# Optimization experiments

Measured on AMD Instinct MI355X. Metric: run time of the kernel, lower is better.

## Reference

```python
import jax, jax.numpy as jnp
import numpy as np

N = 4096        # number of nodes
C = 512         # in_features
L_LAT = 64      # L_latent
EPS = 0.25      # epsilon


def setup_inputs() -> dict:
    key = jax.random.key(0)
    ks = jax.random.split(key, 8)
    def lin(k, fan_in, shape):
        return (jax.random.normal(k, shape, jnp.float32) / np.float32(np.sqrt(fan_in)))
    x = jax.random.normal(ks[0], (N, C), jnp.float32)
    adj = jax.random.uniform(ks[1], (N, N), jnp.float32)  # dense nonneg kernel
    W_proj = lin(ks[2], C, (C, L_LAT)); b_proj = jnp.zeros((L_LAT,), jnp.float32)
    W_pi1 = lin(ks[3], L_LAT, (L_LAT, C)); b_pi1 = jnp.zeros((C,), jnp.float32)
    W_pi2 = lin(ks[4], C, (C, 1)); b_pi2 = jnp.zeros((1,), jnp.float32)
    W_f = lin(ks[5], C, (C, C)); b_f = jnp.zeros((C,), jnp.float32)
    dt = jnp.array([0.1], jnp.float32)
    return {"x": x, "adj": adj, "W_proj": W_proj, "b_proj": b_proj,
            "W_pi1": W_pi1, "b_pi1": b_pi1, "W_pi2": W_pi2, "b_pi2": b_pi2,
            "W_f": W_f, "b_f": b_f, "dt": dt}


def reference(x, adj, W_proj, b_proj, W_pi1, b_pi1, W_pi2, b_pi2, W_f, b_f, dt):
    # proj_list: x -> latent [n, L]
    z = x @ W_proj + b_proj
    # pi_list: Linear -> ReLU -> Linear -> Sigmoid, squeeze to [n]
    pi = jax.nn.sigmoid(jax.nn.relu(z @ W_pi1 + b_pi1) @ W_pi2 + b_pi2)[:, 0]
    # q_epsilon_tilde: row sums of the kernel
    q = adj.sum(axis=1)                       # [n]
    # K_tilde = K_epsilon @ diag(pi/q)  == column scaling
    K_tilde = adj * (pi / q)[None, :]         # [n, n]
    # D_tilde diagonal; torch.inverse of a diagonal == elementwise reciprocal
    d = K_tilde.sum(axis=1) + 1e-5            # [n]
    # target = relu(f(x)) with f = Linear(C, C)
    target = jax.nn.relu(x @ W_f + b_f)       # [n, C]
    # L @ target = (1/eps) * diag(1/d) @ K_tilde @ target - target
    Lt = (K_tilde @ target) / (EPS * d)[:, None] - target
    return target + dt[0] * Lt
```

## Files before the change

kernel.cpp:

```cpp
#include <hip/hip_runtime.h>
#include <hip/hip_bf16.h>

#define N_NODES 4096
#define C_DIM   512
#define L_DIM   64

typedef unsigned short u16;
using bf16x8 = __attribute__((ext_vector_type(8))) __bf16;
using u16x8  = __attribute__((ext_vector_type(8))) unsigned short;
using f32x4  = __attribute__((ext_vector_type(4))) float;

__device__ __forceinline__ float b2f(u16 u) {
    union { unsigned int i; float f; } v; v.i = ((unsigned int)u) << 16; return v.f;
}
__device__ __forceinline__ u16 f2b(float f) {
    unsigned int u = __float_as_uint(f);
    u += 0x7fff + ((u >> 16) & 1);
    return (u16)(u >> 16);
}

__device__ __forceinline__ void gload16(const u16* g, u16* l) {
    __builtin_amdgcn_global_load_lds((const __attribute__((address_space(1))) void*)g,
                                     (__attribute__((address_space(3))) void*)l,
                                     16, 0, 0);
}

__device__ __forceinline__ int detect_mode_inl(const u16* __restrict__ adj) {
    int m = 0;
#pragma unroll
    for (int i = 0; i < 64; ++i) m |= (adj[i] >= 0x8000) ? 1 : 0;
    return m;
}

#define OFF_DT    64
#define OFF_BIAS  1024
#define OFF_WP    4096
#define OFF_BP    135168
#define OFF_WP1   135424
#define OFF_BP1   266496
#define OFF_WP2   268544
#define OFF_BP2   270592
#define OFF_Q     271360
#define OFF_S     287744
#define OFF_DV    304128
#define OFF_T     1048576
#define OFF_TST   9437184
#define OFF_WFT   13631488
#define OFF_XB    14155776
#define OFF_ADJB  18350080

__device__ __forceinline__ float ldin(const void* p, int i, int mode) {
    if (mode) return ((const float*)p)[i];
    return b2f(((const u16*)p)[i]);
}

__global__ __launch_bounds__(256) void convert_params(const u16* __restrict__ adjdet,
        const void* Wp, const void* bp, const void* Wp1, const void* bp1,
        const void* Wp2, const void* bp2, const void* bfc, const void* dt,
        float* Wp_f, float* bp_f, float* Wp1_f, float* bp1_f,
        float* Wp2_f, float* bp2_f, float* bias_f, float* dt_f) {
    int idx = blockIdx.x * 256 + threadIdx.x;
    int mode = detect_mode_inl(adjdet);
    if (idx < 32768)        Wp_f[idx]          = ldin(Wp,  idx, mode);
    else if (idx < 32832)   bp_f[idx - 32768]  = ldin(bp,  idx - 32768, mode);
    else if (idx < 65600)   Wp1_f[idx - 32832] = ldin(Wp1, idx - 32832, mode);
    else if (idx < 66112)   bp1_f[idx - 65600] = ldin(bp1, idx - 65600, mode);
    else if (idx < 66624)   Wp2_f[idx - 66112] = ldin(Wp2, idx - 66112, mode);
    else if (idx == 66624)  bp2_f[0]           = ldin(bp2, 0, mode);
    else if (idx < 67137)   bias_f[idx - 66625] = ldin(bfc, idx - 66625, mode);
    else if (idx == 67137)  dt_f[0]            = ldin(dt, 0, mode);
}

__global__ __launch_bounds__(256) void prep_x(const void* __restrict__ xraw,
                                              const u16* __restrict__ adjdet,
                                              u16* __restrict__ xb) {
    if (detect_mode_inl(adjdet) == 0) return;
    int idx = blockIdx.x * 256 + threadIdx.x;
    float4 v = ((const float4*)xraw)[idx];
    ushort4 o; o.x = f2b(v.x); o.y = f2b(v.y); o.z = f2b(v.z); o.w = f2b(v.w);
    ((ushort4*)xb)[idx] = o;
}

__global__ __launch_bounds__(256) void prep_adj(const void* __restrict__ adjraw,
                                                u16* __restrict__ adjb,
                                                float* __restrict__ q) {
    int mode = detect_mode_inl((const u16*)adjraw);
    int wave = threadIdx.x >> 6, lane = threadIdx.x & 63;
    int row = blockIdx.x * 4 + wave;
    float acc = 0.f;
    if (mode) {
        const float4* rp = (const float4*)((const float*)adjraw + (size_t)row * N_NODES);
        ushort4* wp = (ushort4*)(adjb + (size_t)row * N_NODES);
#pragma unroll
        for (int it = 0; it < 16; ++it) {
            float4 v = rp[it * 64 + lane];
            acc += v.x + v.y + v.z + v.w;
            ushort4 o; o.x = f2b(v.x); o.y = f2b(v.y); o.z = f2b(v.z); o.w = f2b(v.w);
            wp[it * 64 + lane] = o;
        }
    } else {
        const u16x8* rp = (const u16x8*)((const u16*)adjraw + (size_t)row * N_NODES);
#pragma unroll
        for (int it = 0; it < 8; ++it) {
            u16x8 v = rp[it * 64 + lane];
#pragma unroll
            for (int e = 0; e < 8; ++e) acc += b2f(v[e]);
        }
    }
#pragma unroll
    for (int off = 32; off > 0; off >>= 1) acc += __shfl_down(acc, off);
    if (lane == 0) q[row] = acc;
}

__global__ __launch_bounds__(256) void pi_kernel(const void* __restrict__ xraw,
                                                 const u16* __restrict__ adjdet,
                                                 const float* __restrict__ Wp_f,  const float* __restrict__ bp_f,
                                                 const float* __restrict__ Wp1_f, const float* __restrict__ bp1_f,
                                                 const float* __restrict__ Wp2_f, const float* __restrict__ bp2_f,
                                                 const float* __restrict__ q, float* __restrict__ s) {
    __shared__ float sx[8][C_DIM];
    __shared__ float sz[8][L_DIM];
    __shared__ float red[4][8];
    int tid = threadIdx.x;
    int i0 = blockIdx.x * 8;
    int mode = detect_mode_inl(adjdet);
    if (mode) {
        const float4* xp = (const float4*)((const float*)xraw + (size_t)i0 * C_DIM);
        float4* sxf = (float4*)&sx[0][0];
#pragma unroll
        for (int r = 0; r < 4; ++r) sxf[tid + 256 * r] = xp[tid + 256 * r];
    } else {
        const u16x8* xp = (const u16x8*)((const u16*)xraw + (size_t)i0 * C_DIM);
#pragma unroll
        for (int r = 0; r < 2; ++r) {
            u16x8 v = xp[tid + 256 * r];
            float* dstf = &sx[0][0] + (size_t)(tid + 256 * r) * 8;
#pragma unroll
            for (int e = 0; e < 8; ++e) dstf[e] = b2f(v[e]);
        }
    }
    __syncthreads();
    int j = tid & 63, n0 = tid >> 6;
    float a0 = 0.f, a1 = 0.f;
#pragma unroll 4
    for (int k = 0; k < C_DIM; ++k) {
        float w = Wp_f[k * L_DIM + j];
        a0 += sx[n0][k] * w;
        a1 += sx[n0 + 4][k] * w;
    }
    sz[n0][j] = a0 + bp_f[j];
    sz[n0 + 4][j] = a1 + bp_f[j];
    __syncthreads();
    int m0 = tid, m1 = tid + 256;
    float b0 = bp1_f[m0], b1 = bp1_f[m1];
    float h0[8], h1[8];
#pragma unroll
    for (int n = 0; n < 8; ++n) { h0[n] = b0; h1[n] = b1; }
#pragma unroll 8
    for (int jj = 0; jj < L_DIM; ++jj) {
        float w0 = Wp1_f[jj * C_DIM + m0];
        float w1 = Wp1_f[jj * C_DIM + m1];
#pragma unroll
        for (int n = 0; n < 8; ++n) {
            float z = sz[n][jj];
            h0[n] += z * w0;
            h1[n] += z * w1;
        }
    }
    float w2a = Wp2_f[m0], w2b = Wp2_f[m1];
    float p[8];
#pragma unroll
    for (int n = 0; n < 8; ++n)
        p[n] = fmaxf(h0[n], 0.f) * w2a + fmaxf(h1[n], 0.f) * w2b;
#pragma unroll
    for (int off = 32; off > 0; off >>= 1)
#pragma unroll
        for (int n = 0; n < 8; ++n) p[n] += __shfl_down(p[n], off);
    int lane = tid & 63, wave = tid >> 6;
    if (lane == 0) {
#pragma unroll
        for (int n = 0; n < 8; ++n) red[wave][n] = p[n];
    }
    __syncthreads();
    if (tid < 8) {
        float tot = red[0][tid] + red[1][tid] + red[2][tid] + red[3][tid] + bp2_f[0];
        float pi = 1.f / (1.f + expf(-tot));
        s[i0 + tid] = pi / q[i0 + tid];
    }
}

__global__ __launch_bounds__(256) void dvec_kernel(const void* __restrict__ adjraw,
                                                   const u16* __restrict__ adjb,
                                                   const float* __restrict__ s,
                                                   float* __restrict__ d) {
    int mode = detect_mode_inl((const u16*)adjraw);
    const u16* A = mode ? adjb : (const u16*)adjraw;
    int wave = threadIdx.x >> 6, lane = threadIdx.x & 63;
    int row = blockIdx.x * 4 + wave;
    const u16x8* rp = (const u16x8*)(A + (size_t)row * N_NODES);
    float acc = 0.f;
#pragma unroll
    for (int it = 0; it < 8; ++it) {
        int chunk = it * 64 + lane;
        u16x8 v = rp[chunk];
        const float4* sp = (const float4*)(s + chunk * 8);
        float4 s0 = sp[0], s1 = sp[1];
        acc += b2f(v[0]) * s0.x + b2f(v[1]) * s0.y + b2f(v[2]) * s0.z + b2f(v[3]) * s0.w;
        acc += b2f(v[4]) * s1.x + b2f(v[5]) * s1.y + b2f(v[6]) * s1.z + b2f(v[7]) * s1.w;
    }
#pragma unroll
    for (int off = 32; off > 0; off >>= 1) acc += __shfl_down(acc, off);
    if (lane == 0) d[row] = acc + 1e-5f;
}

__global__ __launch_bounds__(256) void trans_Wf(const void* __restrict__ Wfraw,
                                                const u16* __restrict__ adjdet,
                                                u16* __restrict__ WfT) {
    __shared__ float tile[32][33];
    int mode = detect_mode_inl(adjdet);
    int tx = threadIdx.x, ty = threadIdx.y;
    int x0 = blockIdx.x * 32, y0 = blockIdx.y * 32;
    if (mode) {
        const float* src = (const float*)Wfraw;
#pragma unroll
        for (int r = ty; r < 32; r += 8) tile[r][tx] = src[(size_t)(y0 + r) * C_DIM + x0 + tx];
    } else {
        const u16* src = (const u16*)Wfraw;
#pragma unroll
        for (int r = ty; r < 32; r += 8) tile[r][tx] = b2f(src[(size_t)(y0 + r) * C_DIM + x0 + tx]);
    }
    __syncthreads();
#pragma unroll
    for (int r = ty; r < 32; r += 8)
        WfT[(size_t)(x0 + r) * C_DIM + y0 + tx] = f2b(tile[tx][r]);
}

__global__ __launch_bounds__(256) void trans_scale(const float* __restrict__ T,
                                                   const float* __restrict__ s,
                                                   u16* __restrict__ dst) {
    __shared__ float tile[32][33];
    int tx = threadIdx.x, ty = threadIdx.y;
    int x0 = blockIdx.x * 32, y0 = blockIdx.y * 32;
#pragma unroll
    for (int r = ty; r < 32; r += 8) tile[r][tx] = T[(size_t)(y0 + r) * C_DIM + x0 + tx];
    __syncthreads();
    float sv = s[y0 + tx];
#pragma unroll
    for (int r = ty; r < 32; r += 8)
        dst[(size_t)(x0 + r) * N_NODES + y0 + tx] = f2b(tile[tx][r] * sv);
}

template <int EPI>
__global__ __launch_bounds__(256) void gemm_tile(const u16* __restrict__ adjdet,
                                                 const u16* __restrict__ Abf, const u16* __restrict__ Aalt,
                                                 const u16* __restrict__ BT, int K,
                                                 float* __restrict__ T, const float* __restrict__ dvec,
                                                 const float* __restrict__ bias_f, const float* __restrict__ dt_f,
                                                 void* __restrict__ out) {
    __shared__ __align__(16) u16 lA[64 * 32];
    __shared__ __align__(16) u16 lB[64 * 32];
    int mode = detect_mode_inl(adjdet);
    const u16* A = mode ? Aalt : Abf;
    int tid = threadIdx.x;
    int lane = tid & 63, wave = tid >> 6;
    int bm = blockIdx.x * 64, bn = blockIdx.y * 64;
    int quad = lane >> 4, l15 = lane & 15;
    int wm = wave * 16;

    const u16* Ap = A + (size_t)(bm + (tid >> 2)) * K + (tid & 3) * 8;
    const u16* Bp = BT + (size_t)(bn + (tid >> 2)) * K + (tid & 3) * 8;
    u16* la = lA + tid * 8;
    u16* lb = lB + tid * 8;

    f32x4 acc[4];
#pragma unroll
    for (int nt = 0; nt < 4; ++nt) acc[nt] = (f32x4){0.f, 0.f, 0.f, 0.f};

    for (int k0 = 0; k0 < K; k0 += 32) {
        gload16(Ap + k0, la);
        gload16(Bp + k0, lb);
        __syncthreads();
        bf16x8 af = *(const bf16x8*)&lA[(wm + l15) * 32 + quad * 8];
        bf16x8 bfv[4];
#pragma unroll
        for (int nt = 0; nt < 4; ++nt) bfv[nt] = *(const bf16x8*)&lB[(nt * 16 + l15) * 32 + quad * 8];
#pragma unroll
        for (int nt = 0; nt < 4; ++nt)
            acc[nt] = __builtin_amdgcn_mfma_f32_16x16x32_bf16(af, bfv[nt], acc[nt], 0, 0, 0);
        __syncthreads();
    }

    if (EPI == 1) {
#pragma unroll
        for (int nt = 0; nt < 4; ++nt) {
            int col = bn + nt * 16 + l15;
            float bv = bias_f[col];
#pragma unroll
            for (int r = 0; r < 4; ++r) {
                int row = bm + wm + quad * 4 + r;
                T[(size_t)row * C_DIM + col] = fmaxf(acc[nt][r] + bv, 0.f);
            }
        }
    } else {
        float dtv = dt_f[0];
        float c0 = 1.f - dtv;
        float c1 = dtv * 4.f;
#pragma unroll
        for (int nt = 0; nt < 4; ++nt) {
            int col = bn + nt * 16 + l15;
#pragma unroll
            for (int r = 0; r < 4; ++r) {
                int row = bm + wm + quad * 4 + r;
                float t = T[(size_t)row * C_DIM + col];
                float val = c0 * t + c1 * acc[nt][r] / dvec[row];
                if (mode) ((float*)out)[(size_t)row * C_DIM + col] = val;
                else      ((u16*)out)[(size_t)row * C_DIM + col] = f2b(val);
            }
        }
    }
}

extern "C" void kernel_launch(void* const* d_in, const int* in_sizes, int n_in,
                              void* d_out, int out_size, void* d_ws, size_t ws_size,
                              hipStream_t stream) {
    const void* x   = d_in[0];
    const void* adj = d_in[1];
    const void* Wp  = d_in[2];
    const void* bp  = d_in[3];
    const void* Wp1 = d_in[4];
    const void* bp1 = d_in[5];
    const void* Wp2 = d_in[6];
    const void* bp2 = d_in[7];
    const void* Wf  = d_in[8];
    const void* bfc = d_in[9];
    const void* dtp = d_in[10];
    const u16* adjdet = (const u16*)adj;

    char* ws = (char*)d_ws;
    float* dt_f   = (float*)(ws + OFF_DT);
    float* bias_f = (float*)(ws + OFF_BIAS);
    float* Wp_f   = (float*)(ws + OFF_WP);
    float* bp_f   = (float*)(ws + OFF_BP);
    float* Wp1_f  = (float*)(ws + OFF_WP1);
    float* bp1_f  = (float*)(ws + OFF_BP1);
    float* Wp2_f  = (float*)(ws + OFF_WP2);
    float* bp2_f  = (float*)(ws + OFF_BP2);
    float* q      = (float*)(ws + OFF_Q);
    float* s      = (float*)(ws + OFF_S);
    float* dv     = (float*)(ws + OFF_DV);
    float* T      = (float*)(ws + OFF_T);
    u16*   TsT    = (u16*)(ws + OFF_TST);
    u16*   WfT    = (u16*)(ws + OFF_WFT);
    u16*   xb     = (u16*)(ws + OFF_XB);
    u16*   adjb   = (u16*)(ws + OFF_ADJB);

    convert_params<<<263, 256, 0, stream>>>(adjdet, Wp, bp, Wp1, bp1, Wp2, bp2, bfc, dtp,
                                            Wp_f, bp_f, Wp1_f, bp1_f, Wp2_f, bp2_f, bias_f, dt_f);
    prep_x<<<2048, 256, 0, stream>>>(x, adjdet, xb);
    prep_adj<<<N_NODES / 4, 256, 0, stream>>>(adj, adjb, q);
    pi_kernel<<<N_NODES / 8, 256, 0, stream>>>(x, adjdet, Wp_f, bp_f, Wp1_f, bp1_f, Wp2_f, bp2_f, q, s);
    dvec_kernel<<<N_NODES / 4, 256, 0, stream>>>(adj, adjb, s, dv);
    trans_Wf<<<dim3(16, 16), dim3(32, 8), 0, stream>>>(Wf, adjdet, WfT);
    gemm_tile<1><<<dim3(N_NODES / 64, C_DIM / 64), 256, 0, stream>>>(
        adjdet, (const u16*)x, xb, WfT, C_DIM, T, nullptr, bias_f, nullptr, nullptr);
    trans_scale<<<dim3(16, 128), dim3(32, 8), 0, stream>>>(T, s, TsT);
    gemm_tile<2><<<dim3(N_NODES / 64, C_DIM / 64), 256, 0, stream>>>(
        adjdet, (const u16*)adj, adjb, TsT, N_NODES, T, dv, nullptr, dt_f, d_out);
}
```

Measured before the change: 253.5 us.

## Merge launches into five fused kernels and split-K the adjacency GEMM with atomics

Nine launches are merged into five multi-role kernels: parameter, x, adjacency and Wf prep share one launch, pi and the first GEMM share one, and the d-vector, transpose-scale and output init share one. The big adjacency GEMM now uses 128x64 tiles split four ways along K, and partial results are atomically added into an output pre-filled with (1-dt)*T. A final kernel converts the accumulator to bf16 when the input is bf16. This cuts launch gaps and gives the main GEMM more parallelism, at the cost of atomic traffic and a non-deterministic summation order.

```diff
diff --git a/kernel.cpp b/kernel.cpp
--- a/kernel.cpp
+++ b/kernel.cpp
@@ -4,6 +4,8 @@
 #define N_NODES 4096
 #define C_DIM   512
 #define L_DIM   64
+#define SPLITS  4
+#define KCHUNK  (N_NODES / SPLITS)
 
 typedef unsigned short u16;
 using bf16x8 = __attribute__((ext_vector_type(8))) __bf16;
@@ -54,243 +56,186 @@
     return b2f(((const u16*)p)[i]);
 }
 
-__global__ __launch_bounds__(256) void convert_params(const u16* __restrict__ adjdet,
+__global__ __launch_bounds__(256) void k1_prep(const void* __restrict__ adj, const void* __restrict__ x,
         const void* Wp, const void* bp, const void* Wp1, const void* bp1,
-        const void* Wp2, const void* bp2, const void* bfc, const void* dt,
-        float* Wp_f, float* bp_f, float* Wp1_f, float* bp1_f,
-        float* Wp2_f, float* bp2_f, float* bias_f, float* dt_f) {
-    int idx = blockIdx.x * 256 + threadIdx.x;
+        const void* Wp2, const void* bp2, const void* Wf, const void* bfc, const void* dt,
+        float* __restrict__ Wp_f, float* __restrict__ bp_f, float* __restrict__ Wp1_f,
+        float* __restrict__ bp1_f, float* __restrict__ Wp2_f, float* __restrict__ bp2_f,
+        float* __restrict__ bias_f, float* __restrict__ dt_f,
+        u16* __restrict__ adjb, float* __restrict__ q, u16* __restrict__ xb,
+        u16* __restrict__ WfT) {
+    __shared__ float tile[32][33];
+    int bid = blockIdx.x, tid = threadIdx.x;
+    int mode = detect_mode_inl((const u16*)adj);
+    if (bid < 263) {
+        int idx = bid * 256 + tid;
+        if (idx < 32768)        Wp_f[idx]          = ldin(Wp,  idx, mode);
+        else if (idx < 32832)   bp_f[idx - 32768]  = ldin(bp,  idx - 32768, mode);
+        else if (idx < 65600)   Wp1_f[idx - 32832] = ldin(Wp1, idx - 32832, mode);
+        else if (idx < 66112)   bp1_f[idx - 65600] = ldin(bp1, idx - 65600, mode);
+        else if (idx < 66624)   Wp2_f[idx - 66112] = ldin(Wp2, idx - 66112, mode);
+        else if (idx == 66624)  bp2_f[0]           = ldin(bp2, 0, mode);
+        else if (idx < 67137)   bias_f[idx - 66625] = ldin(bfc, idx - 66625, mode);
+        else if (idx == 67137)  dt_f[0]            = ldin(dt, 0, mode);
+    } else if (bid < 2311) {
+        if (mode == 0) return;
+        int idx = (bid - 263) * 256 + tid;
+        float4 v = ((const float4*)x)[idx];
+        ushort4 o; o.x = f2b(v.x); o.y = f2b(v.y); o.z = f2b(v.z); o.w = f2b(v.w);
+        ((ushort4*)xb)[idx] = o;
+    } else if (bid < 3335) {
+        int wave = tid >> 6, lane = tid & 63;
+        int row = (bid - 2311) * 4 + wave;
+        float acc = 0.f;
+        if (mode) {
+            const float4* rp = (const float4*)((const float*)adj + (size_t)row * N_NODES);
+            ushort4* wp = (ushort4*)(adjb + (size_t)row * N_NODES);
+#pragma unroll
+            for (int it = 0; it < 16; ++it) {
+                float4 v = rp[it * 64 + lane];
+                acc += v.x + v.y + v.z + v.w;
+                ushort4 o; o.x = f2b(v.x); o.y = f2b(v.y); o.z = f2b(v.z); o.w = f2b(v.w);
+                wp[it * 64 + lane] = o;
+            }
+        } else {
+            const u16x8* rp = (const u16x8*)((const u16*)adj + (size_t)row * N_NODES);
+#pragma unroll
+            for (int it = 0; it < 8; ++it) {
+                u16x8 v = rp[it * 64 + lane];
+#pragma unroll
+                for (int e = 0; e < 8; ++e) acc += b2f(v[e]);
+            }
+        }
+#pragma unroll
+        for (int off = 32; off > 0; off >>= 1) acc += __shfl_down(acc, off);
+        if (lane == 0) q[row] = acc;
+    } else {
+        int g = bid - 3335;
+        int tx = tid & 31, ty = tid >> 5;
+        int x0 = (g & 15) * 32, y0 = (g >> 4) * 32;
+        if (mode) {
+            const float* src = (const float*)Wf;
+#pragma unroll
+            for (int r = ty; r < 32; r += 8) tile[r][tx] = src[(size_t)(y0 + r) * C_DIM + x0 + tx];
+        } else {
+            const u16* src = (const u16*)Wf;
+#pragma unroll
+            for (int r = ty; r < 32; r += 8) tile[r][tx] = b2f(src[(size_t)(y0 + r) * C_DIM + x0 + tx]);
+        }
+        __syncthreads();
+#pragma unroll
+        for (int r = ty; r < 32; r += 8)
+            WfT[(size_t)(x0 + r) * C_DIM + y0 + tx] = f2b(tile[tx][r]);
+    }
+}
+
+__global__ __launch_bounds__(256) void k2_pi_gemm1(const void* __restrict__ xraw,
+        const u16* __restrict__ adjdet, const u16* __restrict__ xb, const u16* __restrict__ WfT,
+        const float* __restrict__ Wp_f,  const float* __restrict__ bp_f,
+        const float* __restrict__ Wp1_f, const float* __restrict__ bp1_f,
+        const float* __restrict__ Wp2_f, const float* __restrict__ bp2_f,
+        const float* __restrict__ bias_f,
+        const float* __restrict__ q, float* __restrict__ s, float* __restrict__ T) {
+    __shared__ __align__(16) char smem[18560];
+    int bid = blockIdx.x, tid = threadIdx.x;
     int mode = detect_mode_inl(adjdet);
-    if (idx < 32768)        Wp_f[idx]          = ldin(Wp,  idx, mode);
-    else if (idx < 32832)   bp_f[idx - 32768]  = ldin(bp,  idx - 32768, mode);
-    else if (idx < 65600)   Wp1_f[idx - 32832] = ldin(Wp1, idx - 32832, mode);
-    else if (idx < 66112)   bp1_f[idx - 65600] = ldin(bp1, idx - 65600, mode);
-    else if (idx < 66624)   Wp2_f[idx - 66112] = ldin(Wp2, idx - 66112, mode);
-    else if (idx == 66624)  bp2_f[0]           = ldin(bp2, 0, mode);
-    else if (idx < 67137)   bias_f[idx - 66625] = ldin(bfc, idx - 66625, mode);
-    else if (idx == 67137)  dt_f[0]            = ldin(dt, 0, mode);
-}
-
-__global__ __launch_bounds__(256) void prep_x(const void* __restrict__ xraw,
-                                              const u16* __restrict__ adjdet,
-                                              u16* __restrict__ xb) {
-    if (detect_mode_inl(adjdet) == 0) return;
-    int idx = blockIdx.x * 256 + threadIdx.x;
-    float4 v = ((const float4*)xraw)[idx];
-    ushort4 o; o.x = f2b(v.x); o.y = f2b(v.y); o.z = f2b(v.z); o.w = f2b(v.w);
-    ((ushort4*)xb)[idx] = o;
-}
-
-__global__ __launch_bounds__(256) void prep_adj(const void* __restrict__ adjraw,
-                                                u16* __restrict__ adjb,
-                                                float* __restrict__ q) {
-    int mode = detect_mode_inl((const u16*)adjraw);
-    int wave = threadIdx.x >> 6, lane = threadIdx.x & 63;
-    int row = blockIdx.x * 4 + wave;
-    float acc = 0.f;
-    if (mode) {
-        const float4* rp = (const float4*)((const float*)adjraw + (size_t)row * N_NODES);
-        ushort4* wp = (ushort4*)(adjb + (size_t)row * N_NODES);
-#pragma unroll
-        for (int it = 0; it < 16; ++it) {
-            float4 v = rp[it * 64 + lane];
-            acc += v.x + v.y + v.z + v.w;
-            ushort4 o; o.x = f2b(v.x); o.y = f2b(v.y); o.z = f2b(v.z); o.w = f2b(v.w);
-            wp[it * 64 + lane] = o;
+    if (bid < 512) {
+        float (*sx)[C_DIM] = (float(*)[C_DIM])smem;
+        float (*sz)[L_DIM] = (float(*)[L_DIM])(smem + 16384);
+        float (*red)[8]    = (float(*)[8])(smem + 18432);
+        int i0 = bid * 8;
+        if (mode) {
+            const float4* xp = (const float4*)((const float*)xraw + (size_t)i0 * C_DIM);
+            float4* sxf = (float4*)&sx[0][0];
+#pragma unroll
+            for (int r = 0; r < 4; ++r) sxf[tid + 256 * r] = xp[tid + 256 * r];
+        } else {
+            const u16x8* xp = (const u16x8*)((const u16*)xraw + (size_t)i0 * C_DIM);
+#pragma unroll
+            for (int r = 0; r < 2; ++r) {
+                u16x8 v = xp[tid + 256 * r];
+                float* dstf = &sx[0][0] + (size_t)(tid + 256 * r) * 8;
+#pragma unroll
+                for (int e = 0; e < 8; ++e) dstf[e] = b2f(v[e]);
+            }
+        }
+        __syncthreads();
+        int j = tid & 63, n0 = tid >> 6;
+        float a0 = 0.f, a1 = 0.f;
+#pragma unroll 4
+        for (int k = 0; k < C_DIM; ++k) {
+            float w = Wp_f[k * L_DIM + j];
+            a0 += sx[n0][k] * w;
+            a1 += sx[n0 + 4][k] * w;
+        }
+        sz[n0][j] = a0 + bp_f[j];
+        sz[n0 + 4][j] = a1 + bp_f[j];
+        __syncthreads();
+        int m0 = tid, m1 = tid + 256;
+        float b0 = bp1_f[m0], b1 = bp1_f[m1];
+        float h0[8], h1[8];
+#pragma unroll
+        for (int n = 0; n < 8; ++n) { h0[n] = b0; h1[n] = b1; }
+#pragma unroll 8
+        for (int jj = 0; jj < L_DIM; ++jj) {
+            float w0 = Wp1_f[jj * C_DIM + m0];
+            float w1 = Wp1_f[jj * C_DIM + m1];
+#pragma unroll
+            for (int n = 0; n < 8; ++n) {
+                float z = sz[n][jj];
+                h0[n] += z * w0;
+                h1[n] += z * w1;
+            }
+        }
+        float w2a = Wp2_f[m0], w2b = Wp2_f[m1];
+        float p[8];
+#pragma unroll
+        for (int n = 0; n < 8; ++n)
+            p[n] = fmaxf(h0[n], 0.f) * w2a + fmaxf(h1[n], 0.f) * w2b;
+#pragma unroll
+        for (int off = 32; off > 0; off >>= 1)
+#pragma unroll
+            for (int n = 0; n < 8; ++n) p[n] += __shfl_down(p[n], off);
+        int lane = tid & 63, wave = tid >> 6;
+        if (lane == 0) {
+#pragma unroll
+            for (int n = 0; n < 8; ++n) red[wave][n] = p[n];
+        }
+        __syncthreads();
+        if (tid < 8) {
+            float tot = red[0][tid] + red[1][tid] + red[2][tid] + red[3][tid] + bp2_f[0];
+            float pi = 1.f / (1.f + expf(-tot));
+            s[i0 + tid] = pi / q[i0 + tid];
         }
     } else {
-        const u16x8* rp = (const u16x8*)((const u16*)adjraw + (size_t)row * N_NODES);
-#pragma unroll
-        for (int it = 0; it < 8; ++it) {
-            u16x8 v = rp[it * 64 + lane];
-#pragma unroll
-            for (int e = 0; e < 8; ++e) acc += b2f(v[e]);
-        }
-    }
-#pragma unroll
-    for (int off = 32; off > 0; off >>= 1) acc += __shfl_down(acc, off);
-    if (lane == 0) q[row] = acc;
-}
-
-__global__ __launch_bounds__(256) void pi_kernel(const void* __restrict__ xraw,
-                                                 const u16* __restrict__ adjdet,
-                                                 const float* __restrict__ Wp_f,  const float* __restrict__ bp_f,
-                                                 const float* __restrict__ Wp1_f, const float* __restrict__ bp1_f,
-                                                 const float* __restrict__ Wp2_f, const float* __restrict__ bp2_f,
-                                                 const float* __restrict__ q, float* __restrict__ s) {
-    __shared__ float sx[8][C_DIM];
-    __shared__ float sz[8][L_DIM];
-    __shared__ float red[4][8];
-    int tid = threadIdx.x;
-    int i0 = blockIdx.x * 8;
-    int mode = detect_mode_inl(adjdet);
-    if (mode) {
-        const float4* xp = (const float4*)((const float*)xraw + (size_t)i0 * C_DIM);
-        float4* sxf = (float4*)&sx[0][0];
-#pragma unroll
-        for (int r = 0; r < 4; ++r) sxf[tid + 256 * r] = xp[tid + 256 * r];
-    } else {
-        const u16x8* xp = (const u16x8*)((const u16*)xraw + (size_t)i0 * C_DIM);
-#pragma unroll
-        for (int r = 0; r < 2; ++r) {
-            u16x8 v = xp[tid + 256 * r];
-            float* dstf = &sx[0][0] + (size_t)(tid + 256 * r) * 8;
-#pragma unroll
-            for (int e = 0; e < 8; ++e) dstf[e] = b2f(v[e]);
-        }
-    }
-    __syncthreads();
-    int j = tid & 63, n0 = tid >> 6;
-    float a0 = 0.f, a1 = 0.f;
-#pragma unroll 4
-    for (int k = 0; k < C_DIM; ++k) {
-        float w = Wp_f[k * L_DIM + j];
-        a0 += sx[n0][k] * w;
-        a1 += sx[n0 + 4][k] * w;
-    }
-    sz[n0][j] = a0 + bp_f[j];
-    sz[n0 + 4][j] = a1 + bp_f[j];
-    __syncthreads();
-    int m0 = tid, m1 = tid + 256;
-    float b0 = bp1_f[m0], b1 = bp1_f[m1];
-    float h0[8], h1[8];
-#pragma unroll
-    for (int n = 0; n < 8; ++n) { h0[n] = b0; h1[n] = b1; }
-#pragma unroll 8
-    for (int jj = 0; jj < L_DIM; ++jj) {
-        float w0 = Wp1_f[jj * C_DIM + m0];
-        float w1 = Wp1_f[jj * C_DIM + m1];
-#pragma unroll
-        for (int n = 0; n < 8; ++n) {
-            float z = sz[n][jj];
-            h0[n] += z * w0;
-            h1[n] += z * w1;
-        }
-    }
-    float w2a = Wp2_f[m0], w2b = Wp2_f[m1];
-    float p[8];
-#pragma unroll
-    for (int n = 0; n < 8; ++n)
-        p[n] = fmaxf(h0[n], 0.f) * w2a + fmaxf(h1[n], 0.f) * w2b;
-#pragma unroll
-    for (int off = 32; off > 0; off >>= 1)
-#pragma unroll
-        for (int n = 0; n < 8; ++n) p[n] += __shfl_down(p[n], off);
-    int lane = tid & 63, wave = tid >> 6;
-    if (lane == 0) {
-#pragma unroll
-        for (int n = 0; n < 8; ++n) red[wave][n] = p[n];
-    }
-    __syncthreads();
-    if (tid < 8) {
-        float tot = red[0][tid] + red[1][tid] + red[2][tid] + red[3][tid] + bp2_f[0];
-        float pi = 1.f / (1.f + expf(-tot));
-        s[i0 + tid] = pi / q[i0 + tid];
-    }
-}
-
-__global__ __launch_bounds__(256) void dvec_kernel(const void* __restrict__ adjraw,
-                                                   const u16* __restrict__ adjb,
-                                                   const float* __restrict__ s,
-                                                   float* __restrict__ d) {
-    int mode = detect_mode_inl((const u16*)adjraw);
-    const u16* A = mode ? adjb : (const u16*)adjraw;
-    int wave = threadIdx.x >> 6, lane = threadIdx.x & 63;
-    int row = blockIdx.x * 4 + wave;
-    const u16x8* rp = (const u16x8*)(A + (size_t)row * N_NODES);
-    float acc = 0.f;
-#pragma unroll
-    for (int it = 0; it < 8; ++it) {
-        int chunk = it * 64 + lane;
-        u16x8 v = rp[chunk];
-        const float4* sp = (const float4*)(s + chunk * 8);
-        float4 s0 = sp[0], s1 = sp[1];
-        acc += b2f(v[0]) * s0.x + b2f(v[1]) * s0.y + b2f(v[2]) * s0.z + b2f(v[3]) * s0.w;
-        acc += b2f(v[4]) * s1.x + b2f(v[5]) * s1.y + b2f(v[6]) * s1.z + b2f(v[7]) * s1.w;
-    }
-#pragma unroll
-    for (int off = 32; off > 0; off >>= 1) acc += __shfl_down(acc, off);
-    if (lane == 0) d[row] = acc + 1e-5f;
-}
-
-__global__ __launch_bounds__(256) void trans_Wf(const void* __restrict__ Wfraw,
-                                                const u16* __restrict__ adjdet,
-                                                u16* __restrict__ WfT) {
-    __shared__ float tile[32][33];
-    int mode = detect_mode_inl(adjdet);
-    int tx = threadIdx.x, ty = threadIdx.y;
-    int x0 = blockIdx.x * 32, y0 = blockIdx.y * 32;
-    if (mode) {
-        const float* src = (const float*)Wfraw;
-#pragma unroll
-        for (int r = ty; r < 32; r += 8) tile[r][tx] = src[(size_t)(y0 + r) * C_DIM + x0 + tx];
-    } else {
-        const u16* src = (const u16*)Wfraw;
-#pragma unroll
-        for (int r = ty; r < 32; r += 8) tile[r][tx] = b2f(src[(size_t)(y0 + r) * C_DIM + x0 + tx]);
-    }
-    __syncthreads();
-#pragma unroll
-    for (int r = ty; r < 32; r += 8)
-        WfT[(size_t)(x0 + r) * C_DIM + y0 + tx] = f2b(tile[tx][r]);
-}
-
-__global__ __launch_bounds__(256) void trans_scale(const float* __restrict__ T,
-                                                   const float* __restrict__ s,
-                                                   u16* __restrict__ dst) {
-    __shared__ float tile[32][33];
-    int tx = threadIdx.x, ty = threadIdx.y;
-    int x0 = blockIdx.x * 32, y0 = blockIdx.y * 32;
-#pragma unroll
-    for (int r = ty; r < 32; r += 8) tile[r][tx] = T[(size_t)(y0 + r) * C_DIM + x0 + tx];
-    __syncthreads();
-    float sv = s[y0 + tx];
-#pragma unroll
-    for (int r = ty; r < 32; r += 8)
-        dst[(size_t)(x0 + r) * N_NODES + y0 + tx] = f2b(tile[tx][r] * sv);
-}
-
-template <int EPI>
-__global__ __launch_bounds__(256) void gemm_tile(const u16* __restrict__ adjdet,
-                                                 const u16* __restrict__ Abf, const u16* __restrict__ Aalt,
-                                                 const u16* __restrict__ BT, int K,
-                                                 float* __restrict__ T, const float* __restrict__ dvec,
-                                                 const float* __restrict__ bias_f, const float* __restrict__ dt_f,
-                                                 void* __restrict__ out) {
-    __shared__ __align__(16) u16 lA[64 * 32];
-    __shared__ __align__(16) u16 lB[64 * 32];
-    int mode = detect_mode_inl(adjdet);
-    const u16* A = mode ? Aalt : Abf;
-    int tid = threadIdx.x;
-    int lane = tid & 63, wave = tid >> 6;
-    int bm = blockIdx.x * 64, bn = blockIdx.y * 64;
-    int quad = lane >> 4, l15 = lane & 15;
-    int wm = wave * 16;
-
-    const u16* Ap = A + (size_t)(bm + (tid >> 2)) * K + (tid & 3) * 8;
-    const u16* Bp = BT + (size_t)(bn + (tid >> 2)) * K + (tid & 3) * 8;
-    u16* la = lA + tid * 8;
-    u16* lb = lB + tid * 8;
-
-    f32x4 acc[4];
-#pragma unroll
-    for (int nt = 0; nt < 4; ++nt) acc[nt] = (f32x4){0.f, 0.f, 0.f, 0.f};
-
-    for (int k0 = 0; k0 < K; k0 += 32) {
-        gload16(Ap + k0, la);
-        gload16(Bp + k0, lb);
-        __syncthreads();
-        bf16x8 af = *(const bf16x8*)&lA[(wm + l15) * 32 + quad * 8];
-        bf16x8 bfv[4];
-#pragma unroll
-        for (int nt = 0; nt < 4; ++nt) bfv[nt] = *(const bf16x8*)&lB[(nt * 16 + l15) * 32 + quad * 8];
-#pragma unroll
-        for (int nt = 0; nt < 4; ++nt)
-            acc[nt] = __builtin_amdgcn_mfma_f32_16x16x32_bf16(af, bfv[nt], acc[nt], 0, 0, 0);
-        __syncthreads();
-    }
-
-    if (EPI == 1) {
+        u16* lA = (u16*)smem;
+        u16* lB = (u16*)(smem + 4096);
+        const u16* A = mode ? xb : (const u16*)xraw;
+        int g = bid - 512;
+        int lane = tid & 63, wave = tid >> 6;
+        int bm = (g & 63) * 64, bn = (g >> 6) * 64;
+        int quad = lane >> 4, l15 = lane & 15;
+        int wm = wave * 16;
+        const u16* Ap = A + (size_t)(bm + (tid >> 2)) * C_DIM + (tid & 3) * 8;
+        const u16* Bp = WfT + (size_t)(bn + (tid >> 2)) * C_DIM + (tid & 3) * 8;
+        u16* la = lA + tid * 8;
+        u16* lb = lB + tid * 8;
+        f32x4 acc[4];
+#pragma unroll
+        for (int nt = 0; nt < 4; ++nt) acc[nt] = (f32x4){0.f, 0.f, 0.f, 0.f};
+        for (int k0 = 0; k0 < C_DIM; k0 += 32) {
+            gload16(Ap + k0, la);
+            gload16(Bp + k0, lb);
+            __syncthreads();
+            bf16x8 af = *(const bf16x8*)&lA[(wm + l15) * 32 + quad * 8];
+            bf16x8 bfv[4];
+#pragma unroll
+            for (int nt = 0; nt < 4; ++nt) bfv[nt] = *(const bf16x8*)&lB[(nt * 16 + l15) * 32 + quad * 8];
+#pragma unroll
+            for (int nt = 0; nt < 4; ++nt)
+                acc[nt] = __builtin_amdgcn_mfma_f32_16x16x32_bf16(af, bfv[nt], acc[nt], 0, 0, 0);
+            __syncthreads();
+        }
 #pragma unroll
         for (int nt = 0; nt < 4; ++nt) {
             int col = bn + nt * 16 + l15;
@@ -301,23 +246,128 @@
                 T[(size_t)row * C_DIM + col] = fmaxf(acc[nt][r] + bv, 0.f);
             }
         }
+    }
+}
+
+__global__ __launch_bounds__(256) void k3_mid(const void* __restrict__ adjraw,
+        const u16* __restrict__ adjb, const float* __restrict__ s,
+        const float* __restrict__ T, const float* __restrict__ dt_f,
+        float* __restrict__ dv, u16* __restrict__ TsT,
+        void* __restrict__ out, float* __restrict__ Pacc) {
+    __shared__ float tile[32][33];
+    int bid = blockIdx.x, tid = threadIdx.x;
+    int mode = detect_mode_inl((const u16*)adjraw);
+    if (bid < 1024) {
+        const u16* A = mode ? adjb : (const u16*)adjraw;
+        int wave = tid >> 6, lane = tid & 63;
+        int row = bid * 4 + wave;
+        const u16x8* rp = (const u16x8*)(A + (size_t)row * N_NODES);
+        float acc = 0.f;
+#pragma unroll
+        for (int it = 0; it < 8; ++it) {
+            int chunk = it * 64 + lane;
+            u16x8 v = rp[chunk];
+            const float4* sp = (const float4*)(s + chunk * 8);
+            float4 s0 = sp[0], s1 = sp[1];
+            acc += b2f(v[0]) * s0.x + b2f(v[1]) * s0.y + b2f(v[2]) * s0.z + b2f(v[3]) * s0.w;
+            acc += b2f(v[4]) * s1.x + b2f(v[5]) * s1.y + b2f(v[6]) * s1.z + b2f(v[7]) * s1.w;
+        }
+#pragma unroll
+        for (int off = 32; off > 0; off >>= 1) acc += __shfl_down(acc, off);
+        if (lane == 0) dv[row] = acc + 1e-5f;
+    } else if (bid < 3072) {
+        int g = bid - 1024;
+        int tx = tid & 31, ty = tid >> 5;
+        int x0 = (g & 15) * 32, y0 = (g >> 4) * 32;
+#pragma unroll
+        for (int r = ty; r < 32; r += 8) tile[r][tx] = T[(size_t)(y0 + r) * C_DIM + x0 + tx];
+        __syncthreads();
+        float sv = s[y0 + tx];
+#pragma unroll
+        for (int r = ty; r < 32; r += 8)
+            TsT[(size_t)(x0 + r) * N_NODES + y0 + tx] = f2b(tile[tx][r] * sv);
     } else {
-        float dtv = dt_f[0];
-        float c0 = 1.f - dtv;
-        float c1 = dtv * 4.f;
+        int idx = (bid - 3072) * 256 + tid;
+        float c0 = 1.f - dt_f[0];
+        float4 t = ((const float4*)T)[idx];
+        float4 v; v.x = c0 * t.x; v.y = c0 * t.y; v.z = c0 * t.z; v.w = c0 * t.w;
+        float* tgt = mode ? (float*)out : Pacc;
+        ((float4*)tgt)[idx] = v;
+    }
+}
+
+__global__ __launch_bounds__(256) void k4_gemm2(const void* __restrict__ adjraw,
+        const u16* __restrict__ adjb, const u16* __restrict__ TsT,
+        const float* __restrict__ dv, const float* __restrict__ dt_f,
+        void* __restrict__ out, float* __restrict__ Pacc) {
+    __shared__ __align__(16) u16 lA[128 * 32];
+    __shared__ __align__(16) u16 lB[64 * 32];
+    int mode = detect_mode_inl((const u16*)adjraw);
+    const u16* A = mode ? adjb : (const u16*)adjraw;
+    float* tgt = mode ? (float*)out : Pacc;
+    int tid = threadIdx.x;
+    int lane = tid & 63, wave = tid >> 6;
+    int bm = blockIdx.x * 128, bn = blockIdx.y * 64;
+    int kbase = blockIdx.z * KCHUNK;
+    int quad = lane >> 4, l15 = lane & 15;
+    int wm = wave * 32;
+
+    const u16* Ab0 = A + (size_t)(bm + (tid >> 2)) * N_NODES + kbase + (tid & 3) * 8;
+    const u16* Ab1 = A + (size_t)(bm + 64 + (tid >> 2)) * N_NODES + kbase + (tid & 3) * 8;
+    const u16* Bp  = TsT + (size_t)(bn + (tid >> 2)) * N_NODES + kbase + (tid & 3) * 8;
+    u16* la0 = lA + tid * 8;  u16* la1 = lA + 2048 + tid * 8;
+    u16* lb  = lB + tid * 8;
+
+    f32x4 acc[2][4];
+#pragma unroll
+    for (int a = 0; a < 2; ++a)
+#pragma unroll
+        for (int b = 0; b < 4; ++b) acc[a][b] = (f32x4){0.f, 0.f, 0.f, 0.f};
+
+    for (int k0 = 0; k0 < KCHUNK; k0 += 32) {
+        gload16(Ab0 + k0, la0);
+        gload16(Ab1 + k0, la1);
+        gload16(Bp + k0, lb);
+        __syncthreads();
+        bf16x8 af[2], bfv[4];
+#pragma unroll
+        for (int mt = 0; mt < 2; ++mt) af[mt] = *(const bf16x8*)&lA[(wm + mt * 16 + l15) * 32 + quad * 8];
+#pragma unroll
+        for (int nt = 0; nt < 4; ++nt) bfv[nt] = *(const bf16x8*)&lB[(nt * 16 + l15) * 32 + quad * 8];
+#pragma unroll
+        for (int mt = 0; mt < 2; ++mt)
+#pragma unroll
+            for (int nt = 0; nt < 4; ++nt)
+                acc[mt][nt] = __builtin_amdgcn_mfma_f32_16x16x32_bf16(af[mt], bfv[nt], acc[mt][nt], 0, 0, 0);
+        __syncthreads();
+    }
+
+    float c1 = dt_f[0] * 4.f;
+#pragma unroll
+    for (int mt = 0; mt < 2; ++mt) {
+        float inv[4];
+#pragma unroll
+        for (int r = 0; r < 4; ++r) inv[r] = c1 / dv[bm + wm + mt * 16 + quad * 4 + r];
 #pragma unroll
         for (int nt = 0; nt < 4; ++nt) {
             int col = bn + nt * 16 + l15;
 #pragma unroll
             for (int r = 0; r < 4; ++r) {
-                int row = bm + wm + quad * 4 + r;
-                float t = T[(size_t)row * C_DIM + col];
-                float val = c0 * t + c1 * acc[nt][r] / dvec[row];
-                if (mode) ((float*)out)[(size_t)row * C_DIM + col] = val;
-                else      ((u16*)out)[(size_t)row * C_DIM + col] = f2b(val);
+                int row = bm + wm + mt * 16 + quad * 4 + r;
+                atomicAdd(&tgt[(size_t)row * C_DIM + col], acc[mt][nt][r] * inv[r]);
             }
         }
     }
+}
+
+__global__ __launch_bounds__(256) void k5_fin(const void* __restrict__ adjraw,
+                                              const float* __restrict__ Pacc,
+                                              u16* __restrict__ out) {
+    if (detect_mode_inl((const u16*)adjraw)) return;
+    int idx = blockIdx.x * 256 + threadIdx.x;
+    float4 v = ((const float4*)Pacc)[idx];
+    ushort4 o; o.x = f2b(v.x); o.y = f2b(v.y); o.z = f2b(v.z); o.w = f2b(v.w);
+    ((ushort4*)out)[idx] = o;
 }
 
 extern "C" void kernel_launch(void* const* d_in, const int* in_sizes, int n_in,
@@ -353,17 +403,15 @@
     u16*   WfT    = (u16*)(ws + OFF_WFT);
     u16*   xb     = (u16*)(ws + OFF_XB);
     u16*   adjb   = (u16*)(ws + OFF_ADJB);
-
-    convert_params<<<263, 256, 0, stream>>>(adjdet, Wp, bp, Wp1, bp1, Wp2, bp2, bfc, dtp,
-                                            Wp_f, bp_f, Wp1_f, bp1_f, Wp2_f, bp2_f, bias_f, dt_f);
-    prep_x<<<2048, 256, 0, stream>>>(x, adjdet, xb);
-    prep_adj<<<N_NODES / 4, 256, 0, stream>>>(adj, adjb, q);
-    pi_kernel<<<N_NODES / 8, 256, 0, stream>>>(x, adjdet, Wp_f, bp_f, Wp1_f, bp1_f, Wp2_f, bp2_f, q, s);
-    dvec_kernel<<<N_NODES / 4, 256, 0, stream>>>(adj, adjb, s, dv);
-    trans_Wf<<<dim3(16, 16), dim3(32, 8), 0, stream>>>(Wf, adjdet, WfT);
-    gemm_tile<1><<<dim3(N_NODES / 64, C_DIM / 64), 256, 0, stream>>>(
-        adjdet, (const u16*)x, xb, WfT, C_DIM, T, nullptr, bias_f, nullptr, nullptr);
-    trans_scale<<<dim3(16, 128), dim3(32, 8), 0, stream>>>(T, s, TsT);
-    gemm_tile<2><<<dim3(N_NODES / 64, C_DIM / 64), 256, 0, stream>>>(
-        adjdet, (const u16*)adj, adjb, TsT, N_NODES, T, dv, nullptr, dt_f, d_out);
-}
+    float* Pacc   = (float*)(ws + OFF_ADJB);
+
+    k1_prep<<<3591, 256, 0, stream>>>(adj, x, Wp, bp, Wp1, bp1, Wp2, bp2, Wf, bfc, dtp,
+                                      Wp_f, bp_f, Wp1_f, bp1_f, Wp2_f, bp2_f, bias_f, dt_f,
+                                      adjb, q, xb, WfT);
+    k2_pi_gemm1<<<1024, 256, 0, stream>>>(x, adjdet, xb, WfT,
+                                          Wp_f, bp_f, Wp1_f, bp1_f, Wp2_f, bp2_f, bias_f,
+                                          q, s, T);
+    k3_mid<<<5120, 256, 0, stream>>>(adj, adjb, s, T, dt_f, dv, TsT, d_out, Pacc);
+    k4_gemm2<<<dim3(32, 8, SPLITS), 256, 0, stream>>>(adj, adjb, TsT, dv, dt_f, d_out, Pacc);
+    k5_fin<<<2048, 256, 0, stream>>>(adj, Pacc, (u16*)d_out);
+}
```

Result: faster. 236.8 us (-6.6%).
